# Performance work log

Measured on AMD Instinct MI355X. Metric: run time of the kernel, lower is better.

Reference implementation:

```python
import jax, jax.numpy as jnp
import numpy as np

N, E, ND, ED, H, OUT, L, VC = 10000, 160000, 8, 4, 128, 256, 6, 6
HEADS, C = 4, 128  # GATConv: out_channels=128 per head, concat=False -> mean over heads


def _ln(x, g, b, eps=1e-5):
    m = x.mean(-1, keepdims=True)
    v = ((x - m) ** 2).mean(-1, keepdims=True)
    return (x - m) * jax.lax.rsqrt(v + eps) * g + b


def _gat_layer(h, src, dst, e_attr, lw, a_src, a_dst, lew, a_edge, bias):
    # h: [N,H]; e_attr: [Etot,H]; PyG GATConv(heads=4, concat=False, edge_dim=H)
    xh = (h @ lw).reshape(N, HEADS, C)                 # [N,4,128]
    eh = (e_attr @ lew).reshape(-1, HEADS, C)          # [Etot,4,128]
    al_s = jnp.einsum('nhc,hc->nh', xh, a_src)
    al_d = jnp.einsum('nhc,hc->nh', xh, a_dst)
    al_e = jnp.einsum('ehc,hc->eh', eh, a_edge)
    alpha = jax.nn.leaky_relu(al_s[src] + al_d[dst] + al_e, 0.2)  # [Etot,4]
    amax = jax.ops.segment_max(alpha, dst, num_segments=N)
    ex = jnp.exp(alpha - amax[dst])
    den = jax.ops.segment_sum(ex, dst, num_segments=N)
    w = ex / (den[dst] + 1e-16)
    out = jax.ops.segment_sum(xh[src] * w[..., None], dst, num_segments=N)  # [N,4,128]
    return out.mean(axis=1) + bias


def setup_inputs() -> dict:
    key = jax.random.key(0)
    ks = jax.random.split(key, 32)
    s = 0.05
    d = {
        'x': jax.random.normal(ks[0], (N, ND), jnp.float32),
        'edge_index': jax.random.randint(ks[1], (2, E), 0, N),
        'edge_attr': jax.random.uniform(ks[2], (E, ED), jnp.float32),
        'vnf_context': jax.random.normal(ks[3], (1, VC), jnp.float32),
        # node embedding
        'node_w': jax.random.normal(ks[4], (ND, H)) * s, 'node_b': jnp.zeros((H,)),
        # EdgeAttentionLayer
        'ea_proj_w': jax.random.normal(ks[5], (ED, H)) * s, 'ea_proj_b': jnp.zeros((H,)),
        'vnf_w': jax.random.normal(ks[6], (VC, H)) * s, 'vnf_b': jnp.zeros((H,)),
        'att1_w': jax.random.normal(ks[7], (2 * H, H)) * s, 'att1_b': jnp.zeros((H,)),
        'att2_w': jax.random.normal(ks[8], (H, H // 2)) * s, 'att2_b': jnp.zeros((H // 2,)),
        'att3_w': jax.random.normal(ks[9], (H // 2, 1)) * s, 'att3_b': jnp.zeros((1,)),
        # per-layer GATConv params (stacked over L layers)
        'gat_lin_w': jax.random.normal(ks[10], (L, H, HEADS * C)) * s,
        'gat_att_src': jax.random.normal(ks[11], (L, HEADS, C)) * s,
        'gat_att_dst': jax.random.normal(ks[12], (L, HEADS, C)) * s,
        'gat_lin_edge_w': jax.random.normal(ks[13], (L, H, HEADS * C)) * s,
        'gat_att_edge': jax.random.normal(ks[14], (L, HEADS, C)) * s,
        'gat_bias': jnp.zeros((L, C)),
        'ln_scale': jnp.ones((L, H)), 'ln_bias': jnp.zeros((L, H)),
        # output projection
        'out_w': jax.random.normal(ks[15], (H, OUT)) * s, 'out_b': jnp.zeros((OUT,)),
    }
    return d


def reference(x, edge_index, edge_attr, vnf_context, node_w, node_b, ea_proj_w, ea_proj_b,
              vnf_w, vnf_b, att1_w, att1_b, att2_w, att2_b, att3_w, att3_b,
              gat_lin_w, gat_att_src, gat_att_dst, gat_lin_edge_w, gat_att_edge, gat_bias,
              ln_scale, ln_bias, out_w, out_b):
    src, dst = edge_index[0], edge_index[1]
    h = x @ node_w + node_b                                   # [N,128]
    # EdgeAttentionLayer (eval mode, no network_state)
    ef = edge_attr @ ea_proj_w + ea_proj_b                    # [E,128]
    vnf = vnf_context @ vnf_w + vnf_b                         # [1,128]
    comb = jnp.concatenate([ef, jnp.broadcast_to(vnf, (E, H))], axis=-1)
    a = jax.nn.relu(comb @ att1_w + att1_b)
    a = jax.nn.relu(a @ att2_w + att2_b)
    e_gate = jax.nn.sigmoid(a @ att3_w + att3_b)              # [E,1]
    w_edge = ef * e_gate                                      # [E,128]
    # GATConv default add_self_loops=True, fill_value='mean'
    loop = jnp.arange(N)
    src2 = jnp.concatenate([src, loop])
    dst2 = jnp.concatenate([dst, loop])
    e2 = jnp.concatenate([w_edge, jnp.broadcast_to(w_edge.mean(0, keepdims=True), (N, H))], axis=0)
    for l in range(L):
        hc = _gat_layer(h, src2, dst2, e2, gat_lin_w[l], gat_att_src[l], gat_att_dst[l],
                        gat_lin_edge_w[l], gat_att_edge[l], gat_bias[l])
        h = _ln(h + jax.nn.relu(hc), ln_scale[l], ln_bias[l])
    return h @ out_w + out_b                                  # [N,256]
```

## Files before the change

kernel.cpp:

```cpp
#include <hip/hip_runtime.h>
#include <hip/hip_bf16.h>
#include <math.h>

#define Nn 10000
#define Ee 160000
#define ET 170000
#define LL 6

typedef short v8s __attribute__((ext_vector_type(8)));
typedef float v4f __attribute__((ext_vector_type(4)));
typedef float v2f __attribute__((ext_vector_type(2)));

__device__ __forceinline__ unsigned short f2bf(float v) {
    unsigned int b = __float_as_uint(v);
    b += 0x7fffu + ((b >> 16) & 1u);
    return (unsigned short)(b >> 16);
}

__global__ void k_node_embed(const float* __restrict__ x, const float* __restrict__ nw,
                             const float* __restrict__ nb, float* __restrict__ h,
                             unsigned short* __restrict__ hb) {
    int idx = blockIdx.x * 256 + threadIdx.x;
    if (idx >= Nn * 128) return;
    int n = idx >> 7, c = idx & 127;
    const float* xr = x + (size_t)n * 8;
    float acc = nb[c];
#pragma unroll
    for (int k = 0; k < 8; k++) acc += xr[k] * nw[k * 128 + c];
    h[idx] = acc;
    hb[idx] = f2bf(acc);
}

__global__ void k_small(const float* __restrict__ vnfc, const float* __restrict__ vw,
                        const float* __restrict__ vb, const float* __restrict__ eab,
                        const float* __restrict__ a1w, const float* __restrict__ a1b,
                        const float* __restrict__ eaw, float* __restrict__ E1) {
    __shared__ float vr[128];
    __shared__ float sM1[512];
    __shared__ float sd1[128];
    int t = threadIdx.x;
    if (t < 128) {
        float a = vb[t];
#pragma unroll
        for (int k = 0; k < 6; k++) a += vnfc[k] * vw[k * 128 + t];
        vr[t] = a;
    }
    __syncthreads();
    if (t < 128) {
        float a = a1b[t];
        for (int k = 0; k < 128; k++) a += eab[k] * a1w[k * 128 + t];
        for (int k = 0; k < 128; k++) a += vr[k] * a1w[(128 + k) * 128 + t];
        sd1[t] = a;
    }
    {
        int r = t >> 7, j = t & 127;
        float a = 0.f;
        for (int k = 0; k < 128; k++) a += eaw[r * 128 + k] * a1w[k * 128 + j];
        sM1[r * 128 + j] = a;
    }
    __syncthreads();
    if (t < 128) {
        E1[t * 8 + 0] = sM1[t];
        E1[t * 8 + 1] = sM1[128 + t];
        E1[t * 8 + 2] = sM1[256 + t];
        E1[t * 8 + 3] = sM1[384 + t];
        E1[t * 8 + 4] = sd1[t];
        E1[t * 8 + 5] = 0.f; E1[t * 8 + 6] = 0.f; E1[t * 8 + 7] = 0.f;
    }
}

__global__ void k_bmat(const float* __restrict__ glw, const float* __restrict__ gas,
                       const float* __restrict__ gad, const float* __restrict__ glew,
                       const float* __restrict__ gae, float* __restrict__ Bs,
                       float* __restrict__ Bd, float* __restrict__ Be) {
    int idx = blockIdx.x * 256 + threadIdx.x;
    if (idx >= LL * 128 * 4) return;
    int hh = idx & 3, k = (idx >> 2) & 127, l = idx >> 9;
    const float* lwp = glw  + (size_t)l * 65536 + k * 512 + hh * 128;
    const float* lep = glew + (size_t)l * 65536 + k * 512 + hh * 128;
    const float* sp = gas + l * 512 + hh * 128;
    const float* dp = gad + l * 512 + hh * 128;
    const float* ep = gae + l * 512 + hh * 128;
    float s1 = 0, s2 = 0, s3 = 0;
    for (int c = 0; c < 128; c++) {
        float lv = lwp[c];
        s1 += lv * sp[c];
        s2 += lv * dp[c];
        s3 += lep[c] * ep[c];
    }
    Bs[idx] = s1; Bd[idx] = s2; Be[idx] = s3;
}

__global__ void k_glwt(const float* __restrict__ glw, const float* __restrict__ Bs,
                       const float* __restrict__ Bd, unsigned short* __restrict__ glwT) {
    int idx = blockIdx.x * 256 + threadIdx.x;
    if (idx >= LL * 528 * 128) return;
    int k = idx & 127;
    int col = (idx >> 7) % 528;
    int l = idx / (528 * 128);
    float v;
    if (col < 512)      v = glw[(size_t)l * 65536 + k * 512 + col];
    else if (col < 516) v = Bs[l * 512 + k * 4 + (col - 512)];
    else if (col < 520) v = Bd[l * 512 + k * 4 + (col - 516)];
    else                v = 0.f;
    glwT[idx] = f2bf(v);
}

__global__ void k_pb(const float* __restrict__ eaw, const float* __restrict__ eab,
                     const float* __restrict__ Be, float* __restrict__ PB,
                     float* __restrict__ cB) {
    int t = threadIdx.x;
    if (t >= 24) return;
    int l = t >> 2, hh = t & 3;
    const float* bp = Be + l * 512 + hh;
    float s0 = 0, s1 = 0, s2 = 0, s3 = 0, sc = 0;
    for (int k = 0; k < 128; k++) {
        float bv = bp[k * 4];
        s0 += eaw[0 * 128 + k] * bv;
        s1 += eaw[1 * 128 + k] * bv;
        s2 += eaw[2 * 128 + k] * bv;
        s3 += eaw[3 * 128 + k] * bv;
        sc += eab[k] * bv;
    }
    PB[0 * 24 + t] = s0; PB[1 * 24 + t] = s1;
    PB[2 * 24 + t] = s2; PB[3 * 24 + t] = s3;
    cB[t] = sc;
}

__global__ __launch_bounds__(256) void k_edge(
    const float* __restrict__ ea, const float* __restrict__ E1,
    const float* __restrict__ a2w, const float* __restrict__ a2b,
    const float* __restrict__ a3w, const float* __restrict__ a3b,
    const float* __restrict__ PB, const float* __restrict__ cB,
    float* __restrict__ aleT, float* __restrict__ gsum) {
    __shared__ float sw2[128 * 64];
    __shared__ float4 sM[128];
    __shared__ float sD[128];
    __shared__ float prs[4][256];
    __shared__ float gsh[256];
    int t = threadIdx.x;
    int lane = t & 63;
    int p = t >> 6;
    int ps = __builtin_amdgcn_readfirstlane(p);
    for (int z = t; z < 2048; z += 256) ((float4*)sw2)[z] = ((const float4*)a2w)[z];
    if (t < 128) { sM[t] = *(const float4*)(E1 + t * 8); sD[t] = E1[t * 8 + 4]; }
    __syncthreads();
    int eb = blockIdx.x * 256 + lane;
    float4 ev[4];
#pragma unroll
    for (int r = 0; r < 4; r++) ev[r] = *(const float4*)(ea + (size_t)(eb + r * 64) * 4);
    v2f acc[4][8];
#pragma unroll
    for (int j = 0; j < 8; j++) {
        v2f b = {a2b[ps * 16 + 2 * j], a2b[ps * 16 + 2 * j + 1]};
#pragma unroll
        for (int r = 0; r < 4; r++) acc[r][j] = b;
    }
    const float* w2base = sw2 + ps * 16;
    for (int k = 0; k < 128; k++) {
        float4 m = sM[k];
        float dk = sD[k];
        v2f xx[4];
#pragma unroll
        for (int r = 0; r < 4; r++) {
            float xv = fmaxf(dk + ev[r].x * m.x + ev[r].y * m.y + ev[r].z * m.z + ev[r].w * m.w, 0.f);
            xx[r][0] = xv; xx[r][1] = xv;
        }
        const float* w2r = w2base + k * 64;
#pragma unroll
        for (int j4 = 0; j4 < 4; j4++) {
            float4 wv = *(const float4*)(w2r + j4 * 4);
            v2f w01 = {wv.x, wv.y}, w23 = {wv.z, wv.w};
#pragma unroll
            for (int r = 0; r < 4; r++) {
                acc[r][2 * j4]     += xx[r] * w01;
                acc[r][2 * j4 + 1] += xx[r] * w23;
            }
        }
    }
#pragma unroll
    for (int r = 0; r < 4; r++) {
        float pr = 0.f;
#pragma unroll
        for (int j = 0; j < 8; j++) {
            pr += fmaxf(acc[r][j][0], 0.f) * a3w[ps * 16 + 2 * j];
            pr += fmaxf(acc[r][j][1], 0.f) * a3w[ps * 16 + 2 * j + 1];
        }
        prs[p][r * 64 + lane] = pr;
    }
    __syncthreads();
    if (p == 0) {
        float v0 = 0.f, v1 = 0.f, v2 = 0.f, v3 = 0.f, v4 = 0.f;
#pragma unroll
        for (int rep = 0; rep < 4; rep++) {
            int le = rep * 64 + lane;
            float tot = prs[0][le] + prs[1][le] + prs[2][le] + prs[3][le] + a3b[0];
            float g = 1.f / (1.f + __expf(-tot));
            gsh[le] = g;
            float4 evv = ev[rep];
            v0 += g; v1 += g * evv.x; v2 += g * evv.y; v3 += g * evv.z; v4 += g * evv.w;
        }
#pragma unroll
        for (int d = 32; d > 0; d >>= 1) {
            v0 += __shfl_down(v0, d); v1 += __shfl_down(v1, d); v2 += __shfl_down(v2, d);
            v3 += __shfl_down(v3, d); v4 += __shfl_down(v4, d);
        }
        if (lane == 0) {
            atomicAdd(&gsum[0], v0); atomicAdd(&gsum[1], v1); atomicAdd(&gsum[2], v2);
            atomicAdd(&gsum[3], v3); atomicAdd(&gsum[4], v4);
        }
    }
    __syncthreads();
#pragma unroll
    for (int rep = 0; rep < 2; rep++) {
        int i4 = (rep == 0) ? ps : (ps < 2 ? ps + 4 : -1);
        if (i4 >= 0) {
            float4 c  = *(const float4*)(cB + i4 * 4);
            float4 p0 = *(const float4*)(PB + 0 * 24 + i4 * 4);
            float4 p1 = *(const float4*)(PB + 1 * 24 + i4 * 4);
            float4 p2 = *(const float4*)(PB + 2 * 24 + i4 * 4);
            float4 p3 = *(const float4*)(PB + 3 * 24 + i4 * 4);
#pragma unroll
            for (int r = 0; r < 4; r++) {
                float g = gsh[r * 64 + lane];
                float4 evv = ev[r];
                float4 o;
                o.x = g * (c.x + evv.x * p0.x + evv.y * p1.x + evv.z * p2.x + evv.w * p3.x);
                o.y = g * (c.y + evv.x * p0.y + evv.y * p1.y + evv.z * p2.y + evv.w * p3.y);
                o.z = g * (c.z + evv.x * p0.z + evv.y * p1.z + evv.z * p2.z + evv.w * p3.z);
                o.w = g * (c.w + evv.x * p0.w + evv.y * p1.w + evv.z * p2.w + evv.w * p3.w);
                *(float4*)(aleT + (size_t)i4 * Ee * 4 + (size_t)(eb + r * 64) * 4) = o;
            }
        }
    }
}

__global__ void k_lale(const float* __restrict__ gsum, const float* __restrict__ PB,
                       const float* __restrict__ cB, float* __restrict__ lale) {
    int t = threadIdx.x;
    if (t >= 24) return;
    float s = gsum[0] * cB[t] + gsum[1] * PB[t] + gsum[2] * PB[24 + t]
            + gsum[3] * PB[48 + t] + gsum[4] * PB[72 + t];
    lale[t] = s * (1.0f / Ee);
}

__global__ void k_hist(const int* __restrict__ ei, int* __restrict__ hist) {
    int i = blockIdx.x * 256 + threadIdx.x;
    if (i >= ET) return;
    int d = (i < Ee) ? ei[Ee + i] : (i - Ee);
    atomicAdd(&hist[d], 1);
}

__global__ __launch_bounds__(1024) void k_scan(const int* __restrict__ hist,
                                               int* __restrict__ seg, int* __restrict__ pos) {
    __shared__ int wsums[16];
    __shared__ int carry_s;
    int t = threadIdx.x;
    int lane = t & 63, wid = t >> 6;
    if (t == 0) { carry_s = 0; seg[0] = 0; }
    __syncthreads();
    for (int base = 0; base < Nn; base += 1024) {
        int idx = base + t;
        int v = (idx < Nn) ? hist[idx] : 0;
        int sc = v;
#pragma unroll
        for (int d = 1; d < 64; d <<= 1) {
            int up = __shfl_up(sc, d);
            if (lane >= d) sc += up;
        }
        if (lane == 63) wsums[wid] = sc;
        __syncthreads();
        if (wid == 0) {
            int wv = (lane < 16) ? wsums[lane] : 0;
            int wsc = wv;
#pragma unroll
            for (int d = 1; d < 16; d <<= 1) {
                int up = __shfl_up(wsc, d);
                if (lane >= d) wsc += up;
            }
            if (lane < 16) wsums[lane] = wsc - wv;
        }
        __syncthreads();
        int carry = carry_s;
        int inc = sc + wsums[wid] + carry;
        if (idx < Nn) { seg[idx + 1] = inc; pos[idx] = inc - v; }
        __syncthreads();
        if (t == 1023) carry_s = inc;
        __syncthreads();
    }
}

__global__ void k_scatter(const int* __restrict__ ei, int* __restrict__ pos,
                          int2* __restrict__ pse) {
    int i = blockIdx.x * 256 + threadIdx.x;
    if (i >= ET) return;
    int s, d;
    if (i < Ee) { s = ei[i]; d = ei[Ee + i]; } else { s = d = i - Ee; }
    int idx = atomicAdd(&pos[d], 1);
    pse[idx] = make_int2(s, i);
}

__global__ __launch_bounds__(256) void k_xh_mfma(
    const unsigned short* __restrict__ hb, const unsigned short* __restrict__ glwT_l,
    unsigned short* __restrict__ xhb, float* __restrict__ als, float* __restrict__ ald) {
    int t = threadIdx.x;
    int lane = t & 63;
    int w = t >> 6;
    int n0 = blockIdx.x * 16;
    int m = lane & 15, q = lane >> 4;
    v8s fa[4];
    const unsigned short* arow = hb + (size_t)(n0 + m) * 128 + q * 8;
#pragma unroll
    for (int ks = 0; ks < 4; ks++) fa[ks] = *(const v8s*)(arow + ks * 32);
    int nt0 = w * 8;
#pragma unroll
    for (int nt = 0; nt < 8; nt++) {
        int col = (nt0 + nt) * 16 + m;
        const unsigned short* brow = glwT_l + (size_t)col * 128 + q * 8;
        v4f acc = {0.f, 0.f, 0.f, 0.f};
#pragma unroll
        for (int ks = 0; ks < 4; ks++) {
            v8s fb = *(const v8s*)(brow + ks * 32);
            acc = __builtin_amdgcn_mfma_f32_16x16x32_bf16(fa[ks], fb, acc, 0, 0, 0);
        }
#pragma unroll
        for (int r = 0; r < 4; r++)
            xhb[(size_t)(n0 + q * 4 + r) * 512 + col] = f2bf(acc[r]);
    }
    if (w == 3) {
        int col = 512 + m;
        const unsigned short* brow = glwT_l + (size_t)col * 128 + q * 8;
        v4f acc = {0.f, 0.f, 0.f, 0.f};
#pragma unroll
        for (int ks = 0; ks < 4; ks++) {
            v8s fb = *(const v8s*)(brow + ks * 32);
            acc = __builtin_amdgcn_mfma_f32_16x16x32_bf16(fa[ks], fb, acc, 0, 0, 0);
        }
        if (m < 8) {
#pragma unroll
            for (int r = 0; r < 4; r++) {
                int row = n0 + q * 4 + r;
                if (m < 4) als[row * 4 + m] = acc[r];
                else       ald[row * 4 + (m - 4)] = acc[r];
            }
        }
    }
}

__global__ __launch_bounds__(256) void k_agg(
    const int2* __restrict__ pse, const int* __restrict__ seg,
    const float* __restrict__ als, const float* __restrict__ ald,
    const float* __restrict__ aleT_l, const float* __restrict__ lale_l,
    const unsigned short* __restrict__ xhb, const float* __restrict__ bias,
    const float* __restrict__ lnsc, const float* __restrict__ lnbi,
    float* __restrict__ hio, unsigned short* __restrict__ hb) {
    __shared__ float lgS[2][512];
    __shared__ int srcS[2][128];
    __shared__ float msS[2][2][8];
    __shared__ float part[2][128];
    int t = threadIdx.x;
    int lane = t & 63;
    int wv = (t >> 6) & 1;
    int w = t >> 7;
    int n = blockIdx.x * 2 + w;
    int start = seg[n], end = seg[n + 1];
    int deg = end - start;
    int half = (deg + 1) >> 1;
    int s0 = start + wv * half;
    int e0 = wv ? end : start + half;
    int h1 = lane & 3;
    float llh1 = lale_l[h1];
    float a1d = ald[n * 4 + h1];
    float m = -INFINITY, ss = 0.f;
    for (int i = s0 + (lane >> 2); i < e0; i += 16) {
        int idx = i - start;
        int2 se = pse[i];
        float alev = se.y < Ee ? aleT_l[(size_t)se.y * 4 + h1] : llh1;
        float av = als[se.x * 4 + h1] + a1d + alev;
        av = av > 0.f ? av : 0.2f * av;
        if (idx < 128) {
            lgS[w][idx * 4 + h1] = av;
            if (h1 == 0) srcS[w][idx] = se.x;
        }
        if (av > m) { ss = ss * __expf(m - av) + 1.f; m = av; }
        else ss += __expf(av - m);
    }
#pragma unroll
    for (int d = 4; d <= 32; d <<= 1) {
        float mo = __shfl_xor(m, d), so = __shfl_xor(ss, d);
        float mm = fmaxf(m, mo);
        float sv = 0.f;
        if (m > -INFINITY) sv += ss * __expf(m - mm);
        if (mo > -INFINITY) sv += so * __expf(mo - mm);
        m = mm; ss = sv;
    }
    if (lane < 4) { msS[w][wv][lane] = m; msS[w][wv][4 + lane] = ss; }
    __syncthreads();
    {
        float mo = msS[w][1 - wv][h1], so = msS[w][1 - wv][4 + h1];
        float mm = fmaxf(m, mo);
        float sv = 0.f;
        if (m > -INFINITY) sv += ss * __expf(m - mm);
        if (mo > -INFINITY) sv += so * __expf(mo - mm);
        m = mm; ss = sv;
    }
    float mh0 = __shfl(m, 0), mh1 = __shfl(m, 1), mh2 = __shfl(m, 2), mh3 = __shfl(m, 3);
    float iv0 = 1.f / (__shfl(ss, 0) + 1e-16f), iv1 = 1.f / (__shfl(ss, 1) + 1e-16f);
    float iv2 = 1.f / (__shfl(ss, 2) + 1e-16f), iv3 = 1.f / (__shfl(ss, 3) + 1e-16f);
    int lo = wv * half;
    int hi = min(wv ? deg : half, 128);
    for (int z = lo + lane; z < hi; z += 64) {
        float4 lg = *(float4*)&lgS[w][z * 4];
        lg.x = __expf(lg.x - mh0) * iv0;
        lg.y = __expf(lg.y - mh1) * iv1;
        lg.z = __expf(lg.z - mh2) * iv2;
        lg.w = __expf(lg.w - mh3) * iv3;
        *(float4*)&lgS[w][z * 4] = lg;
    }
    int hp = lane >> 4;
    int c8 = lane * 8;
    float4 acc0 = make_float4(0.f, 0.f, 0.f, 0.f);
    float4 acc1 = make_float4(0.f, 0.f, 0.f, 0.f);
    int i2 = lo;
    for (; i2 + 2 <= hi; i2 += 2) {
        int sa = srcS[w][i2], sb = srcS[w][i2 + 1];
        float wg0 = lgS[w][i2 * 4 + hp], wg1 = lgS[w][i2 * 4 + 4 + hp];
        uint4 u0 = *(const uint4*)(xhb + (size_t)sa * 512 + c8);
        uint4 u1 = *(const uint4*)(xhb + (size_t)sb * 512 + c8);
        acc0.x += wg0 * __uint_as_float(u0.x << 16) + wg1 * __uint_as_float(u1.x << 16);
        acc0.y += wg0 * __uint_as_float(u0.x & 0xffff0000u) + wg1 * __uint_as_float(u1.x & 0xffff0000u);
        acc0.z += wg0 * __uint_as_float(u0.y << 16) + wg1 * __uint_as_float(u1.y << 16);
        acc0.w += wg0 * __uint_as_float(u0.y & 0xffff0000u) + wg1 * __uint_as_float(u1.y & 0xffff0000u);
        acc1.x += wg0 * __uint_as_float(u0.z << 16) + wg1 * __uint_as_float(u1.z << 16);
        acc1.y += wg0 * __uint_as_float(u0.z & 0xffff0000u) + wg1 * __uint_as_float(u1.z & 0xffff0000u);
        acc1.z += wg0 * __uint_as_float(u0.w << 16) + wg1 * __uint_as_float(u1.w << 16);
        acc1.w += wg0 * __uint_as_float(u0.w & 0xffff0000u) + wg1 * __uint_as_float(u1.w & 0xffff0000u);
    }
    if (i2 < hi) {
        int sa = srcS[w][i2];
        float wg0 = lgS[w][i2 * 4 + hp];
        uint4 u0 = *(const uint4*)(xhb + (size_t)sa * 512 + c8);
        acc0.x += wg0 * __uint_as_float(u0.x << 16);
        acc0.y += wg0 * __uint_as_float(u0.x & 0xffff0000u);
        acc0.z += wg0 * __uint_as_float(u0.y << 16);
        acc0.w += wg0 * __uint_as_float(u0.y & 0xffff0000u);
        acc1.x += wg0 * __uint_as_float(u0.z << 16);
        acc1.y += wg0 * __uint_as_float(u0.z & 0xffff0000u);
        acc1.z += wg0 * __uint_as_float(u0.w << 16);
        acc1.w += wg0 * __uint_as_float(u0.w & 0xffff0000u);
    }
    float mhp = hp == 0 ? mh0 : hp == 1 ? mh1 : hp == 2 ? mh2 : mh3;
    float ivp = hp == 0 ? iv0 : hp == 1 ? iv1 : hp == 2 ? iv2 : iv3;
    for (int i = start + max(lo, 128); i < e0; i++) {
        int2 se = pse[i];
        float alev = se.y < Ee ? aleT_l[(size_t)se.y * 4 + hp] : lale_l[hp];
        float av = als[se.x * 4 + hp] + ald[n * 4 + hp] + alev;
        av = av > 0.f ? av : 0.2f * av;
        float wg0 = __expf(av - mhp) * ivp;
        uint4 u0 = *(const uint4*)(xhb + (size_t)se.x * 512 + c8);
        acc0.x += wg0 * __uint_as_float(u0.x << 16);
        acc0.y += wg0 * __uint_as_float(u0.x & 0xffff0000u);
        acc0.z += wg0 * __uint_as_float(u0.y << 16);
        acc0.w += wg0 * __uint_as_float(u0.y & 0xffff0000u);
        acc1.x += wg0 * __uint_as_float(u0.z << 16);
        acc1.y += wg0 * __uint_as_float(u0.z & 0xffff0000u);
        acc1.z += wg0 * __uint_as_float(u0.w << 16);
        acc1.w += wg0 * __uint_as_float(u0.w & 0xffff0000u);
    }
#pragma unroll
    for (int d = 16; d <= 32; d <<= 1) {
        acc0.x += __shfl_xor(acc0.x, d); acc0.y += __shfl_xor(acc0.y, d);
        acc0.z += __shfl_xor(acc0.z, d); acc0.w += __shfl_xor(acc0.w, d);
        acc1.x += __shfl_xor(acc1.x, d); acc1.y += __shfl_xor(acc1.y, d);
        acc1.z += __shfl_xor(acc1.z, d); acc1.w += __shfl_xor(acc1.w, d);
    }
    int cc = (lane & 15) * 8;
    if (wv == 1 && lane < 16) {
        *(float4*)&part[w][cc] = acc0;
        *(float4*)&part[w][cc + 4] = acc1;
    }
    __syncthreads();
    if (wv == 0) {
        float4 p0 = *(const float4*)&part[w][cc];
        float4 p1 = *(const float4*)&part[w][cc + 4];
        acc0.x += p0.x; acc0.y += p0.y; acc0.z += p0.z; acc0.w += p0.w;
        acc1.x += p1.x; acc1.y += p1.y; acc1.z += p1.z; acc1.w += p1.w;
        float4 b0 = *(const float4*)(bias + cc), b1 = *(const float4*)(bias + cc + 4);
        float4 h0 = *(const float4*)(hio + (size_t)n * 128 + cc);
        float4 h1v = *(const float4*)(hio + (size_t)n * 128 + cc + 4);
        float4 v0, v1;
        v0.x = h0.x + fmaxf(0.25f * acc0.x + b0.x, 0.f);
        v0.y = h0.y + fmaxf(0.25f * acc0.y + b0.y, 0.f);
        v0.z = h0.z + fmaxf(0.25f * acc0.z + b0.z, 0.f);
        v0.w = h0.w + fmaxf(0.25f * acc0.w + b0.w, 0.f);
        v1.x = h1v.x + fmaxf(0.25f * acc1.x + b1.x, 0.f);
        v1.y = h1v.y + fmaxf(0.25f * acc1.y + b1.y, 0.f);
        v1.z = h1v.z + fmaxf(0.25f * acc1.z + b1.z, 0.f);
        v1.w = h1v.w + fmaxf(0.25f * acc1.w + b1.w, 0.f);
        float s1 = v0.x + v0.y + v0.z + v0.w + v1.x + v1.y + v1.z + v1.w;
        float s2 = v0.x * v0.x + v0.y * v0.y + v0.z * v0.z + v0.w * v0.w
                 + v1.x * v1.x + v1.y * v1.y + v1.z * v1.z + v1.w * v1.w;
#pragma unroll
        for (int d = 1; d <= 8; d <<= 1) {
            s1 += __shfl_xor(s1, d); s2 += __shfl_xor(s2, d);
        }
        float mean = s1 * (1.f / 128.f);
        float var = s2 * (1.f / 128.f) - mean * mean;
        float rinv = rsqrtf(var + 1e-5f);
        if (lane < 16) {
            float4 ls0 = *(const float4*)(lnsc + cc), ls1 = *(const float4*)(lnsc + cc + 4);
            float4 lb0 = *(const float4*)(lnbi + cc), lb1 = *(const float4*)(lnbi + cc + 4);
            float4 o0, o1;
            o0.x = (v0.x - mean) * rinv * ls0.x + lb0.x;
            o0.y = (v0.y - mean) * rinv * ls0.y + lb0.y;
            o0.z = (v0.z - mean) * rinv * ls0.z + lb0.z;
            o0.w = (v0.w - mean) * rinv * ls0.w + lb0.w;
            o1.x = (v1.x - mean) * rinv * ls1.x + lb1.x;
            o1.y = (v1.y - mean) * rinv * ls1.y + lb1.y;
            o1.z = (v1.z - mean) * rinv * ls1.z + lb1.z;
            o1.w = (v1.w - mean) * rinv * ls1.w + lb1.w;
            *(float4*)(hio + (size_t)n * 128 + cc) = o0;
            *(float4*)(hio + (size_t)n * 128 + cc + 4) = o1;
            ushort4 q0, q1;
            q0.x = f2bf(o0.x); q0.y = f2bf(o0.y); q0.z = f2bf(o0.z); q0.w = f2bf(o0.w);
            q1.x = f2bf(o1.x); q1.y = f2bf(o1.y); q1.z = f2bf(o1.z); q1.w = f2bf(o1.w);
            *(ushort4*)(hb + (size_t)n * 128 + cc) = q0;
            *(ushort4*)(hb + (size_t)n * 128 + cc + 4) = q1;
        }
    }
}

__global__ __launch_bounds__(256) void k_out(
    const float* __restrict__ h, const float* __restrict__ ow,
    const float* __restrict__ ob, float* __restrict__ out) {
    __shared__ float4 hs4[8][32];
    int t = threadIdx.x;
    int n0 = blockIdx.x * 8;
    if (t < 256) {
        int i = t >> 5, kb = t & 31;
        hs4[i][kb] = *(const float4*)(h + (size_t)(n0 + i) * 128 + 4 * kb);
    }
    __syncthreads();
    float acc[8] = {0, 0, 0, 0, 0, 0, 0, 0};
    for (int kb = 0; kb < 32; kb++) {
        float w0 = ow[(4 * kb + 0) * 256 + t];
        float w1 = ow[(4 * kb + 1) * 256 + t];
        float w2 = ow[(4 * kb + 2) * 256 + t];
        float w3 = ow[(4 * kb + 3) * 256 + t];
#pragma unroll
        for (int i = 0; i < 8; i++) {
            float4 hv = hs4[i][kb];
            acc[i] += hv.x * w0 + hv.y * w1 + hv.z * w2 + hv.w * w3;
        }
    }
    float b = ob[t];
#pragma unroll
    for (int i = 0; i < 8; i++) out[(size_t)(n0 + i) * 256 + t] = acc[i] + b;
}

extern "C" void kernel_launch(void* const* d_in, const int* in_sizes, int n_in,
                              void* d_out, int out_size, void* d_ws, size_t ws_size,
                              hipStream_t stream) {
    const float* x    = (const float*)d_in[0];
    const int*   ei   = (const int*)d_in[1];
    const float* ea   = (const float*)d_in[2];
    const float* vnfc = (const float*)d_in[3];
    const float* nw   = (const float*)d_in[4];
    const float* nb   = (const float*)d_in[5];
    const float* eaw  = (const float*)d_in[6];
    const float* eab  = (const float*)d_in[7];
    const float* vw   = (const float*)d_in[8];
    const float* vb   = (const float*)d_in[9];
    const float* a1w  = (const float*)d_in[10];
    const float* a1b  = (const float*)d_in[11];
    const float* a2w  = (const float*)d_in[12];
    const float* a2b  = (const float*)d_in[13];
    const float* a3w  = (const float*)d_in[14];
    const float* a3b  = (const float*)d_in[15];
    const float* glw  = (const float*)d_in[16];
    const float* gas  = (const float*)d_in[17];
    const float* gad  = (const float*)d_in[18];
    const float* glew = (const float*)d_in[19];
    const float* gae  = (const float*)d_in[20];
    const float* gb   = (const float*)d_in[21];
    const float* lnsc = (const float*)d_in[22];
    const float* lnbi = (const float*)d_in[23];
    const float* ow   = (const float*)d_in[24];
    const float* ob   = (const float*)d_in[25];
    float* out = (float*)d_out;

    char* w = (char*)d_ws;
    size_t o = 0;
    auto allocf = [&](size_t cnt) { float* p = (float*)(w + o); o += ((cnt * 4 + 255) / 256) * 256; return p; };
    auto alloci = [&](size_t cnt) { int* p = (int*)(w + o); o += ((cnt * 4 + 255) / 256) * 256; return p; };
    auto allocu = [&](size_t cnt) { unsigned short* p = (unsigned short*)(w + o); o += ((cnt * 2 + 255) / 256) * 256; return p; };
    float* h      = allocf((size_t)Nn * 128);
    unsigned short* hb   = allocu((size_t)Nn * 128);
    unsigned short* xhb  = allocu((size_t)Nn * 512);
    unsigned short* glwT = allocu((size_t)LL * 528 * 128);
    float* als    = allocf((size_t)Nn * 4);
    float* ald    = allocf((size_t)Nn * 4);
    float* aleT   = allocf((size_t)LL * Ee * 4);
    float* Bs     = allocf(3072);
    float* Bd     = allocf(3072);
    float* Be     = allocf(3072);
    float* E1     = allocf(1024);
    float* PB     = allocf(96);
    float* cB     = allocf(24);
    float* gsum   = allocf(8);
    float* lale   = allocf(32);
    int* seg  = alloci(Nn + 1);
    int* hist = alloci(Nn);
    int* pos  = alloci(Nn);
    int2* pse = (int2*)alloci((size_t)ET * 2);

    hipMemsetAsync(hist, 0, Nn * sizeof(int), stream);
    hipMemsetAsync(gsum, 0, 8 * sizeof(float), stream);

    k_node_embed<<<(Nn * 128 + 255) / 256, 256, 0, stream>>>(x, nw, nb, h, hb);
    k_small<<<1, 512, 0, stream>>>(vnfc, vw, vb, eab, a1w, a1b, eaw, E1);
    k_bmat<<<(LL * 128 * 4 + 255) / 256, 256, 0, stream>>>(glw, gas, gad, glew, gae, Bs, Bd, Be);
    k_glwt<<<(LL * 528 * 128 + 255) / 256, 256, 0, stream>>>(glw, Bs, Bd, glwT);
    k_pb<<<1, 32, 0, stream>>>(eaw, eab, Be, PB, cB);
    k_edge<<<Ee / 256, 256, 0, stream>>>(ea, E1, a2w, a2b, a3w, a3b, PB, cB, aleT, gsum);
    k_hist<<<(ET + 255) / 256, 256, 0, stream>>>(ei, hist);
    k_scan<<<1, 1024, 0, stream>>>(hist, seg, pos);
    k_scatter<<<(ET + 255) / 256, 256, 0, stream>>>(ei, pos, pse);
    k_lale<<<1, 32, 0, stream>>>(gsum, PB, cB, lale);
    for (int l = 0; l < LL; l++) {
        k_xh_mfma<<<Nn / 16, 256, 0, stream>>>(hb, glwT + (size_t)l * 528 * 128, xhb, als, ald);
        k_agg<<<Nn / 2, 256, 0, stream>>>(pse, seg, als, ald, aleT + (size_t)l * Ee * 4,
                                          lale + l * 4, xhb,
                                          gb + l * 128, lnsc + l * 128, lnbi + l * 128, h, hb);
    }
    k_out<<<Nn / 8, 256, 0, stream>>>(h, ow, ob, out);
}
```

Baseline: 569.6 us.

## Aggregate raw node features before projection, apply head-mean weight after gather

Instead of projecting h to 512-wide per-head features and then gathering those per edge, the layer now gathers 128-wide bf16 h rows weighted per head into a 512-wide aggregate. It then multiplies by a head-stacked weight pre-scaled by 0.25 via MFMA in a new post kernel that also fuses bias, ReLU, residual and LayerNorm. Attention logits come from a separate small kernel that dots h with the precomputed Bs/Bd vectors. This cuts per-edge gather bytes fourfold but adds one launch per layer and a larger K=512 GEMM, and logits are now computed from the fp32 h rather than the bf16 copy.

```diff
diff --git a/kernel.cpp b/kernel.cpp
--- a/kernel.cpp
+++ b/kernel.cpp
@@ -91,19 +91,14 @@
     Bs[idx] = s1; Bd[idx] = s2; Be[idx] = s3;
 }
 
-__global__ void k_glwt(const float* __restrict__ glw, const float* __restrict__ Bs,
-                       const float* __restrict__ Bd, unsigned short* __restrict__ glwT) {
+__global__ void k_wsum(const float* __restrict__ glw, unsigned short* __restrict__ WsumT) {
     int idx = blockIdx.x * 256 + threadIdx.x;
-    if (idx >= LL * 528 * 128) return;
-    int k = idx & 127;
-    int col = (idx >> 7) % 528;
-    int l = idx / (528 * 128);
-    float v;
-    if (col < 512)      v = glw[(size_t)l * 65536 + k * 512 + col];
-    else if (col < 516) v = Bs[l * 512 + k * 4 + (col - 512)];
-    else if (col < 520) v = Bd[l * 512 + k * 4 + (col - 516)];
-    else                v = 0.f;
-    glwT[idx] = f2bf(v);
+    if (idx >= LL * 128 * 512) return;
+    int kk = idx & 511;
+    int c = (idx >> 9) & 127;
+    int l = idx >> 16;
+    float v = 0.25f * glw[(size_t)l * 65536 + (size_t)(kk & 127) * 512 + (kk >> 7) * 128 + c];
+    WsumT[(size_t)l * 65536 + (size_t)c * 512 + kk] = f2bf(v);
 }
 
 __global__ void k_pb(const float* __restrict__ eaw, const float* __restrict__ eab,
@@ -300,64 +295,35 @@
     pse[idx] = make_int2(s, i);
 }
 
-__global__ __launch_bounds__(256) void k_xh_mfma(
-    const unsigned short* __restrict__ hb, const unsigned short* __restrict__ glwT_l,
-    unsigned short* __restrict__ xhb, float* __restrict__ als, float* __restrict__ ald) {
-    int t = threadIdx.x;
-    int lane = t & 63;
-    int w = t >> 6;
-    int n0 = blockIdx.x * 16;
-    int m = lane & 15, q = lane >> 4;
-    v8s fa[4];
-    const unsigned short* arow = hb + (size_t)(n0 + m) * 128 + q * 8;
-#pragma unroll
-    for (int ks = 0; ks < 4; ks++) fa[ks] = *(const v8s*)(arow + ks * 32);
-    int nt0 = w * 8;
-#pragma unroll
-    for (int nt = 0; nt < 8; nt++) {
-        int col = (nt0 + nt) * 16 + m;
-        const unsigned short* brow = glwT_l + (size_t)col * 128 + q * 8;
-        v4f acc = {0.f, 0.f, 0.f, 0.f};
-#pragma unroll
-        for (int ks = 0; ks < 4; ks++) {
-            v8s fb = *(const v8s*)(brow + ks * 32);
-            acc = __builtin_amdgcn_mfma_f32_16x16x32_bf16(fa[ks], fb, acc, 0, 0, 0);
-        }
-#pragma unroll
-        for (int r = 0; r < 4; r++)
-            xhb[(size_t)(n0 + q * 4 + r) * 512 + col] = f2bf(acc[r]);
-    }
-    if (w == 3) {
-        int col = 512 + m;
-        const unsigned short* brow = glwT_l + (size_t)col * 128 + q * 8;
-        v4f acc = {0.f, 0.f, 0.f, 0.f};
-#pragma unroll
-        for (int ks = 0; ks < 4; ks++) {
-            v8s fb = *(const v8s*)(brow + ks * 32);
-            acc = __builtin_amdgcn_mfma_f32_16x16x32_bf16(fa[ks], fb, acc, 0, 0, 0);
-        }
-        if (m < 8) {
-#pragma unroll
-            for (int r = 0; r < 4; r++) {
-                int row = n0 + q * 4 + r;
-                if (m < 4) als[row * 4 + m] = acc[r];
-                else       ald[row * 4 + (m - 4)] = acc[r];
-            }
-        }
-    }
-}
-
-__global__ __launch_bounds__(256) void k_agg(
+__global__ void k_ab(const float* __restrict__ h, const float* __restrict__ Bs_l,
+                     const float* __restrict__ Bd_l, float* __restrict__ als,
+                     float* __restrict__ ald) {
+    int idx = blockIdx.x * 256 + threadIdx.x;
+    if (idx >= Nn * 8) return;
+    int n = idx >> 3, slot = idx & 7;
+    const float* B = (slot < 4) ? Bs_l : Bd_l;
+    int hh = slot & 3;
+    const float4* hr = (const float4*)(h + (size_t)n * 128);
+    float s = 0.f;
+#pragma unroll 8
+    for (int kb = 0; kb < 32; kb++) {
+        float4 hv = hr[kb];
+        s += hv.x * B[(4 * kb + 0) * 4 + hh] + hv.y * B[(4 * kb + 1) * 4 + hh]
+           + hv.z * B[(4 * kb + 2) * 4 + hh] + hv.w * B[(4 * kb + 3) * 4 + hh];
+    }
+    if (slot < 4) als[n * 4 + hh] = s;
+    else          ald[n * 4 + hh] = s;
+}
+
+__global__ __launch_bounds__(256) void k_agg2(
     const int2* __restrict__ pse, const int* __restrict__ seg,
     const float* __restrict__ als, const float* __restrict__ ald,
     const float* __restrict__ aleT_l, const float* __restrict__ lale_l,
-    const unsigned short* __restrict__ xhb, const float* __restrict__ bias,
-    const float* __restrict__ lnsc, const float* __restrict__ lnbi,
-    float* __restrict__ hio, unsigned short* __restrict__ hb) {
+    const unsigned short* __restrict__ hb, unsigned short* __restrict__ aggb) {
     __shared__ float lgS[2][512];
     __shared__ int srcS[2][128];
     __shared__ float msS[2][2][8];
-    __shared__ float part[2][128];
+    __shared__ float part[2][512];
     int t = threadIdx.x;
     int lane = t & 63;
     int wv = (t >> 6) & 1;
@@ -418,15 +384,15 @@
         *(float4*)&lgS[w][z * 4] = lg;
     }
     int hp = lane >> 4;
-    int c8 = lane * 8;
+    int cch = (lane & 15) * 8;
     float4 acc0 = make_float4(0.f, 0.f, 0.f, 0.f);
     float4 acc1 = make_float4(0.f, 0.f, 0.f, 0.f);
     int i2 = lo;
     for (; i2 + 2 <= hi; i2 += 2) {
         int sa = srcS[w][i2], sb = srcS[w][i2 + 1];
         float wg0 = lgS[w][i2 * 4 + hp], wg1 = lgS[w][i2 * 4 + 4 + hp];
-        uint4 u0 = *(const uint4*)(xhb + (size_t)sa * 512 + c8);
-        uint4 u1 = *(const uint4*)(xhb + (size_t)sb * 512 + c8);
+        uint4 u0 = *(const uint4*)(hb + (size_t)sa * 128 + cch);
+        uint4 u1 = *(const uint4*)(hb + (size_t)sb * 128 + cch);
         acc0.x += wg0 * __uint_as_float(u0.x << 16) + wg1 * __uint_as_float(u1.x << 16);
         acc0.y += wg0 * __uint_as_float(u0.x & 0xffff0000u) + wg1 * __uint_as_float(u1.x & 0xffff0000u);
         acc0.z += wg0 * __uint_as_float(u0.y << 16) + wg1 * __uint_as_float(u1.y << 16);
@@ -439,7 +405,7 @@
     if (i2 < hi) {
         int sa = srcS[w][i2];
         float wg0 = lgS[w][i2 * 4 + hp];
-        uint4 u0 = *(const uint4*)(xhb + (size_t)sa * 512 + c8);
+        uint4 u0 = *(const uint4*)(hb + (size_t)sa * 128 + cch);
         acc0.x += wg0 * __uint_as_float(u0.x << 16);
         acc0.y += wg0 * __uint_as_float(u0.x & 0xffff0000u);
         acc0.z += wg0 * __uint_as_float(u0.y << 16);
@@ -457,7 +423,7 @@
         float av = als[se.x * 4 + hp] + ald[n * 4 + hp] + alev;
         av = av > 0.f ? av : 0.2f * av;
         float wg0 = __expf(av - mhp) * ivp;
-        uint4 u0 = *(const uint4*)(xhb + (size_t)se.x * 512 + c8);
+        uint4 u0 = *(const uint4*)(hb + (size_t)se.x * 128 + cch);
         acc0.x += wg0 * __uint_as_float(u0.x << 16);
         acc0.y += wg0 * __uint_as_float(u0.x & 0xffff0000u);
         acc0.z += wg0 * __uint_as_float(u0.y << 16);
@@ -467,65 +433,82 @@
         acc1.z += wg0 * __uint_as_float(u0.w << 16);
         acc1.w += wg0 * __uint_as_float(u0.w & 0xffff0000u);
     }
-#pragma unroll
-    for (int d = 16; d <= 32; d <<= 1) {
-        acc0.x += __shfl_xor(acc0.x, d); acc0.y += __shfl_xor(acc0.y, d);
-        acc0.z += __shfl_xor(acc0.z, d); acc0.w += __shfl_xor(acc0.w, d);
-        acc1.x += __shfl_xor(acc1.x, d); acc1.y += __shfl_xor(acc1.y, d);
-        acc1.z += __shfl_xor(acc1.z, d); acc1.w += __shfl_xor(acc1.w, d);
-    }
-    int cc = (lane & 15) * 8;
-    if (wv == 1 && lane < 16) {
-        *(float4*)&part[w][cc] = acc0;
-        *(float4*)&part[w][cc + 4] = acc1;
+    if (wv == 1) {
+        *(float4*)&part[w][lane * 8] = acc0;
+        *(float4*)&part[w][lane * 8 + 4] = acc1;
     }
     __syncthreads();
     if (wv == 0) {
-        float4 p0 = *(const float4*)&part[w][cc];
-        float4 p1 = *(const float4*)&part[w][cc + 4];
+        float4 p0 = *(const float4*)&part[w][lane * 8];
+        float4 p1 = *(const float4*)&part[w][lane * 8 + 4];
         acc0.x += p0.x; acc0.y += p0.y; acc0.z += p0.z; acc0.w += p0.w;
         acc1.x += p1.x; acc1.y += p1.y; acc1.z += p1.z; acc1.w += p1.w;
-        float4 b0 = *(const float4*)(bias + cc), b1 = *(const float4*)(bias + cc + 4);
-        float4 h0 = *(const float4*)(hio + (size_t)n * 128 + cc);
-        float4 h1v = *(const float4*)(hio + (size_t)n * 128 + cc + 4);
-        float4 v0, v1;
-        v0.x = h0.x + fmaxf(0.25f * acc0.x + b0.x, 0.f);
-        v0.y = h0.y + fmaxf(0.25f * acc0.y + b0.y, 0.f);
-        v0.z = h0.z + fmaxf(0.25f * acc0.z + b0.z, 0.f);
-        v0.w = h0.w + fmaxf(0.25f * acc0.w + b0.w, 0.f);
-        v1.x = h1v.x + fmaxf(0.25f * acc1.x + b1.x, 0.f);
-        v1.y = h1v.y + fmaxf(0.25f * acc1.y + b1.y, 0.f);
-        v1.z = h1v.z + fmaxf(0.25f * acc1.z + b1.z, 0.f);
-        v1.w = h1v.w + fmaxf(0.25f * acc1.w + b1.w, 0.f);
-        float s1 = v0.x + v0.y + v0.z + v0.w + v1.x + v1.y + v1.z + v1.w;
-        float s2 = v0.x * v0.x + v0.y * v0.y + v0.z * v0.z + v0.w * v0.w
-                 + v1.x * v1.x + v1.y * v1.y + v1.z * v1.z + v1.w * v1.w;
-#pragma unroll
-        for (int d = 1; d <= 8; d <<= 1) {
-            s1 += __shfl_xor(s1, d); s2 += __shfl_xor(s2, d);
-        }
-        float mean = s1 * (1.f / 128.f);
-        float var = s2 * (1.f / 128.f) - mean * mean;
+        ushort4 q0, q1;
+        q0.x = f2bf(acc0.x); q0.y = f2bf(acc0.y); q0.z = f2bf(acc0.z); q0.w = f2bf(acc0.w);
+        q1.x = f2bf(acc1.x); q1.y = f2bf(acc1.y); q1.z = f2bf(acc1.z); q1.w = f2bf(acc1.w);
+        *(ushort4*)(aggb + (size_t)n * 512 + lane * 8) = q0;
+        *(ushort4*)(aggb + (size_t)n * 512 + lane * 8 + 4) = q1;
+    }
+}
+
+__global__ __launch_bounds__(256) void k_post(
+    const unsigned short* __restrict__ aggb, const unsigned short* __restrict__ WsumT_l,
+    const float* __restrict__ gbias, const float* __restrict__ lnsc,
+    const float* __restrict__ lnbi, float* __restrict__ h,
+    unsigned short* __restrict__ hb) {
+    int t = threadIdx.x;
+    int lane = t & 63, w = t >> 6;
+    int n0 = (blockIdx.x * 4 + w) * 16;
+    if (n0 >= Nn) return;
+    int m = lane & 15, q = lane >> 4;
+    v4f acc[8];
+#pragma unroll
+    for (int nt = 0; nt < 8; nt++) acc[nt] = (v4f){0.f, 0.f, 0.f, 0.f};
+    const unsigned short* arow = aggb + (size_t)(n0 + m) * 512 + q * 8;
+#pragma unroll 4
+    for (int ks = 0; ks < 16; ks++) {
+        v8s fa = *(const v8s*)(arow + ks * 32);
+#pragma unroll
+        for (int nt = 0; nt < 8; nt++) {
+            int col = nt * 16 + m;
+            v8s fb = *(const v8s*)(WsumT_l + (size_t)col * 512 + ks * 32 + q * 8);
+            acc[nt] = __builtin_amdgcn_mfma_f32_16x16x32_bf16(fa, fb, acc[nt], 0, 0, 0);
+        }
+    }
+    float v[8][4];
+    float s1[4] = {0.f, 0.f, 0.f, 0.f}, s2[4] = {0.f, 0.f, 0.f, 0.f};
+#pragma unroll
+    for (int nt = 0; nt < 8; nt++) {
+        int col = nt * 16 + m;
+        float b = gbias[col];
+#pragma unroll
+        for (int r = 0; r < 4; r++) {
+            int row = n0 + q * 4 + r;
+            float val = h[(size_t)row * 128 + col] + fmaxf(acc[nt][r] + b, 0.f);
+            v[nt][r] = val;
+            s1[r] += val; s2[r] += val * val;
+        }
+    }
+#pragma unroll
+    for (int d = 1; d <= 8; d <<= 1) {
+#pragma unroll
+        for (int r = 0; r < 4; r++) {
+            s1[r] += __shfl_xor(s1[r], d);
+            s2[r] += __shfl_xor(s2[r], d);
+        }
+    }
+#pragma unroll
+    for (int r = 0; r < 4; r++) {
+        float mean = s1[r] * (1.f / 128.f);
+        float var = s2[r] * (1.f / 128.f) - mean * mean;
         float rinv = rsqrtf(var + 1e-5f);
-        if (lane < 16) {
-            float4 ls0 = *(const float4*)(lnsc + cc), ls1 = *(const float4*)(lnsc + cc + 4);
-            float4 lb0 = *(const float4*)(lnbi + cc), lb1 = *(const float4*)(lnbi + cc + 4);
-            float4 o0, o1;
-            o0.x = (v0.x - mean) * rinv * ls0.x + lb0.x;
-            o0.y = (v0.y - mean) * rinv * ls0.y + lb0.y;
-            o0.z = (v0.z - mean) * rinv * ls0.z + lb0.z;
-            o0.w = (v0.w - mean) * rinv * ls0.w + lb0.w;
-            o1.x = (v1.x - mean) * rinv * ls1.x + lb1.x;
-            o1.y = (v1.y - mean) * rinv * ls1.y + lb1.y;
-            o1.z = (v1.z - mean) * rinv * ls1.z + lb1.z;
-            o1.w = (v1.w - mean) * rinv * ls1.w + lb1.w;
-            *(float4*)(hio + (size_t)n * 128 + cc) = o0;
-            *(float4*)(hio + (size_t)n * 128 + cc + 4) = o1;
-            ushort4 q0, q1;
-            q0.x = f2bf(o0.x); q0.y = f2bf(o0.y); q0.z = f2bf(o0.z); q0.w = f2bf(o0.w);
-            q1.x = f2bf(o1.x); q1.y = f2bf(o1.y); q1.z = f2bf(o1.z); q1.w = f2bf(o1.w);
-            *(ushort4*)(hb + (size_t)n * 128 + cc) = q0;
-            *(ushort4*)(hb + (size_t)n * 128 + cc + 4) = q1;
+        int row = n0 + q * 4 + r;
+#pragma unroll
+        for (int nt = 0; nt < 8; nt++) {
+            int col = nt * 16 + m;
+            float o = (v[nt][r] - mean) * rinv * lnsc[col] + lnbi[col];
+            h[(size_t)row * 128 + col] = o;
+            hb[(size_t)row * 128 + col] = f2bf(o);
         }
     }
 }
@@ -595,9 +578,9 @@
     auto alloci = [&](size_t cnt) { int* p = (int*)(w + o); o += ((cnt * 4 + 255) / 256) * 256; return p; };
     auto allocu = [&](size_t cnt) { unsigned short* p = (unsigned short*)(w + o); o += ((cnt * 2 + 255) / 256) * 256; return p; };
     float* h      = allocf((size_t)Nn * 128);
-    unsigned short* hb   = allocu((size_t)Nn * 128);
-    unsigned short* xhb  = allocu((size_t)Nn * 512);
-    unsigned short* glwT = allocu((size_t)LL * 528 * 128);
+    unsigned short* hb    = allocu((size_t)Nn * 128);
+    unsigned short* aggb  = allocu((size_t)Nn * 512);
+    unsigned short* WsumT = allocu((size_t)LL * 128 * 512);
     float* als    = allocf((size_t)Nn * 4);
     float* ald    = allocf((size_t)Nn * 4);
     float* aleT   = allocf((size_t)LL * Ee * 4);
@@ -620,7 +603,7 @@
     k_node_embed<<<(Nn * 128 + 255) / 256, 256, 0, stream>>>(x, nw, nb, h, hb);
     k_small<<<1, 512, 0, stream>>>(vnfc, vw, vb, eab, a1w, a1b, eaw, E1);
     k_bmat<<<(LL * 128 * 4 + 255) / 256, 256, 0, stream>>>(glw, gas, gad, glew, gae, Bs, Bd, Be);
-    k_glwt<<<(LL * 528 * 128 + 255) / 256, 256, 0, stream>>>(glw, Bs, Bd, glwT);
+    k_wsum<<<(LL * 128 * 512 + 255) / 256, 256, 0, stream>>>(glw, WsumT);
     k_pb<<<1, 32, 0, stream>>>(eaw, eab, Be, PB, cB);
     k_edge<<<Ee / 256, 256, 0, stream>>>(ea, E1, a2w, a2b, a3w, a3b, PB, cB, aleT, gsum);
     k_hist<<<(ET + 255) / 256, 256, 0, stream>>>(ei, hist);
@@ -628,10 +611,12 @@
     k_scatter<<<(ET + 255) / 256, 256, 0, stream>>>(ei, pos, pse);
     k_lale<<<1, 32, 0, stream>>>(gsum, PB, cB, lale);
     for (int l = 0; l < LL; l++) {
-        k_xh_mfma<<<Nn / 16, 256, 0, stream>>>(hb, glwT + (size_t)l * 528 * 128, xhb, als, ald);
-        k_agg<<<Nn / 2, 256, 0, stream>>>(pse, seg, als, ald, aleT + (size_t)l * Ee * 4,
-                                          lale + l * 4, xhb,
-                                          gb + l * 128, lnsc + l * 128, lnbi + l * 128, h, hb);
+        k_ab<<<(Nn * 8 + 255) / 256, 256, 0, stream>>>(h, Bs + l * 512, Bd + l * 512, als, ald);
+        k_agg2<<<Nn / 2, 256, 0, stream>>>(pse, seg, als, ald, aleT + (size_t)l * Ee * 4,
+                                           lale + l * 4, hb, aggb);
+        k_post<<<(625 + 3) / 4, 256, 0, stream>>>(aggb, WsumT + (size_t)l * 65536,
+                                                  gb + l * 128, lnsc + l * 128, lnbi + l * 128,
+                                                  h, hb);
     }
     k_out<<<Nn / 8, 256, 0, stream>>>(h, ow, ob, out);
 }
```

New measurement: 575.6 us. Within noise of the previous version (+1.0%).
